# Kernel tuning notes

Measured on AMD Instinct MI355X. Metric: run time of the kernel, lower is better.

The kernel has to match this reference:

```python
import jax, jax.numpy as jnp
import numpy as np

D_MODEL = 1024
D_STATE = 64
HEADDIM = 64
EXPAND = 2
D_INNER = D_MODEL * EXPAND          # 2048
NHEADS = D_INNER // HEADDIM          # 32
D_IN_PROJ = 2 * D_INNER + 2 * D_STATE + NHEADS  # 4256
BATCH, SEQLEN = 4, 4096


def layernorm(x, w, b, eps=1e-5):
    mu = jnp.mean(x, axis=-1, keepdims=True)
    var = jnp.mean(jnp.square(x - mu), axis=-1, keepdims=True)
    return (x - mu) * jax.lax.rsqrt(var + eps) * w + b


def setup_inputs() -> dict:
    key = jax.random.key(0)
    ks = jax.random.split(key, 5)
    x = jax.random.normal(ks[0], (BATCH, SEQLEN, D_MODEL), dtype=jnp.float32)
    # xavier-ish small init (gain 0.5) as in _init_weights
    in_proj_w = jax.random.normal(ks[1], (D_IN_PROJ, D_MODEL), dtype=jnp.float32) * 0.5 * np.sqrt(2.0 / (D_IN_PROJ + D_MODEL))
    out_proj_w = jax.random.normal(ks[2], (D_MODEL, D_INNER), dtype=jnp.float32) * 0.5 * np.sqrt(2.0 / (D_MODEL + D_INNER))
    A_log = jnp.log(jnp.arange(1, NHEADS + 1, dtype=jnp.float32))
    dt_bias = jax.random.normal(ks[3], (NHEADS,), dtype=jnp.float32) * 0.01 + 0.1
    Dparam = jnp.ones((NHEADS,), dtype=jnp.float32)
    return {
        'x': x, 'in_proj_w': in_proj_w, 'out_proj_w': out_proj_w,
        'A_log': A_log, 'dt_bias': dt_bias, 'Dparam': Dparam,
        'ln_w': jnp.ones((D_INNER,), jnp.float32), 'ln_b': jnp.zeros((D_INNER,), jnp.float32),
        'ni_w': jnp.ones((D_MODEL,), jnp.float32), 'ni_b': jnp.zeros((D_MODEL,), jnp.float32),
        'no_w': jnp.ones((D_MODEL,), jnp.float32), 'no_b': jnp.zeros((D_MODEL,), jnp.float32),
    }


def _selective_scan(x_multi, A, Bm, Cm, dt):
    # x_multi: [B,L,H,P], A: [H], Bm/Cm: [B,L,N], dt: [B,L,H]
    Bb, L, H, P = x_multi.shape
    N = Bm.shape[-1]
    dA = jnp.minimum(jnp.exp(dt * A[None, None, :]), 0.99)  # [B,L,H]

    def step(h, inp):
        x_t, B_t, C_t, dA_t = inp  # [B,H,P], [B,N], [B,N], [B,H]
        dBx = jnp.einsum('bhp,bn->bhpn', x_t, B_t)
        h = jnp.clip(dA_t[:, :, None, None] * h + dBx, -10.0, 10.0)
        y_t = jnp.einsum('bn,bhpn->bhp', C_t, h)
        return h, y_t

    h0 = jnp.zeros((Bb, H, P, N), dtype=x_multi.dtype)
    xs = (jnp.moveaxis(x_multi, 1, 0), jnp.moveaxis(Bm, 1, 0),
          jnp.moveaxis(Cm, 1, 0), jnp.moveaxis(dA, 1, 0))
    _, y = jax.lax.scan(step, h0, xs)  # y: [L,B,H,P]
    return jnp.moveaxis(y, 0, 1)


def reference(x, in_proj_w, out_proj_w, A_log, dt_bias, Dparam,
              ln_w, ln_b, ni_w, ni_b, no_w, no_b):
    Bb, L, Dm = x.shape
    x_norm = layernorm(x, ni_w, ni_b)
    zxbcdt = jnp.einsum('bld,ed->ble', x_norm, in_proj_w)  # [B,L,D_IN_PROJ]
    z = zxbcdt[..., :D_INNER]
    x_ssm = zxbcdt[..., D_INNER:2 * D_INNER]
    Bm = zxbcdt[..., 2 * D_INNER:2 * D_INNER + D_STATE]
    Cm = zxbcdt[..., 2 * D_INNER + D_STATE:2 * D_INNER + 2 * D_STATE]
    dt = zxbcdt[..., 2 * D_INNER + 2 * D_STATE:]
    dt = jnp.clip(jax.nn.softplus(dt + dt_bias[None, None, :]), 0.001, 0.1)  # [B,L,H]
    A = -jnp.exp(A_log)  # [H]
    x_multi = x_ssm.reshape(Bb, L, NHEADS, HEADDIM)
    y = _selective_scan(x_multi, A, Bm, Cm, dt)  # [B,L,H,P]
    y = y + x_multi * Dparam[None, None, :, None]  # D skip
    y = y.reshape(Bb, L, D_INNER)
    y = y * jax.nn.silu(z)
    y = layernorm(y, ln_w, ln_b)
    y = jnp.einsum('ble,de->bld', y, out_proj_w)
    y = jnp.clip(y, -10.0, 10.0)
    y = layernorm(y, no_w, no_b)
    return y
```

## Files before the change

### kernel.cpp

```cpp
#include <hip/hip_runtime.h>
#include <hip/hip_bf16.h>
#include <stdint.h>

typedef _Float16 F16;
typedef F16 f16x8 __attribute__((ext_vector_type(8)));
typedef F16 f16x4 __attribute__((ext_vector_type(4)));
typedef float f32x4 __attribute__((ext_vector_type(4)));

#define NTOK   16384
#define DMODEL 1024
#define DINNER 2048
#define DSTATE 64
#define NHEADS 32
#define DINPRJ 4256
#define SEQLEN_ 4096
#define SEGLEN 128
#define NSEG   32

__device__ __forceinline__ void load_lds16(const void* g, void* l) {
  __builtin_amdgcn_global_load_lds((__attribute__((address_space(1))) void*)g,
                                   (__attribute__((address_space(3))) void*)l,
                                   16, 0, 0);
}

__device__ __forceinline__ void lds_st8(F16* base, int row, int col, int rowbytes, f16x8 v) {
  int by = (row * rowbytes + col * 2) ^ ((row & 7) << 4);
  *(f16x8*)((char*)base + by) = v;
}
__device__ __forceinline__ void lds_st1(F16* base, int row, int col, int rowbytes, F16 v) {
  int by = (row * rowbytes + col * 2) ^ ((row & 7) << 4);
  *(F16*)((char*)base + by) = v;
}
__device__ __forceinline__ f16x8 lds_ld8(const F16* base, int row, int col, int rowbytes) {
  int by = (row * rowbytes + col * 2) ^ ((row & 7) << 4);
  return *(const f16x8*)((const char*)base + by);
}

__global__ __launch_bounds__(256) void cvt_kernel(const float* __restrict__ src,
                                                  F16* __restrict__ dst, int n4) {
  int i = blockIdx.x * 256 + threadIdx.x;
  if (i >= n4) return;
  float4 v = *(const float4*)(src + (size_t)i * 4);
  f16x4 o = { (F16)v.x, (F16)v.y, (F16)v.z, (F16)v.w };
  *(f16x4*)(dst + (size_t)i * 4) = o;
}

__device__ __forceinline__ void blk_reduce2(float& s, float& ss) {
  __shared__ float red[8];
#pragma unroll
  for (int m = 32; m >= 1; m >>= 1) { s += __shfl_xor(s, m, 64); ss += __shfl_xor(ss, m, 64); }
  int tid = threadIdx.x, wv = tid >> 6;
  if ((tid & 63) == 0) { red[wv * 2] = s; red[wv * 2 + 1] = ss; }
  __syncthreads();
  s  = red[0] + red[2] + red[4] + red[6];
  ss = red[1] + red[3] + red[5] + red[7];
}

__global__ __launch_bounds__(256) void ln_in_kernel(const float* __restrict__ x,
                                                    const float* __restrict__ w,
                                                    const float* __restrict__ b,
                                                    F16* __restrict__ out) {
  int row = blockIdx.x, tid = threadIdx.x;
  const float* xr = x + (size_t)row * DMODEL + tid * 4;
  float4 v = *(const float4*)xr;
  float s = v.x + v.y + v.z + v.w;
  float ss = v.x * v.x + v.y * v.y + v.z * v.z + v.w * v.w;
  blk_reduce2(s, ss);
  float mu = s * (1.f / DMODEL);
  float var = ss * (1.f / DMODEL) - mu * mu;
  float rs = rsqrtf(var + 1e-5f);
  float4 wv = *(const float4*)(w + tid * 4);
  float4 bv = *(const float4*)(b + tid * 4);
  f16x4 o;
  o.x = (F16)((v.x - mu) * rs * wv.x + bv.x);
  o.y = (F16)((v.y - mu) * rs * wv.y + bv.y);
  o.z = (F16)((v.z - mu) * rs * wv.z + bv.z);
  o.w = (F16)((v.w - mu) * rs * wv.w + bv.w);
  *(f16x4*)(out + (size_t)row * DMODEL + tid * 4) = o;
}

template<int KD, int EPI>
__global__ __launch_bounds__(256)
void gemm_kernel(const F16* __restrict__ A, const F16* __restrict__ W, int Nw,
                 F16* __restrict__ Z, F16* __restrict__ XS,
                 float* __restrict__ BC, float* __restrict__ DT,
                 float* __restrict__ O1)
{
  __shared__ __align__(16) F16 Alds[128 * 32];
  __shared__ __align__(16) F16 Blds[128 * 32];
  const int tid = threadIdx.x;
  const int lane = tid & 63;
  const int wid = tid >> 6;
  const int wm = wid >> 1, wn = wid & 1;
  const int m0 = blockIdx.x * 128, n0 = blockIdx.y * 128;
  const int lr = lane & 15, lk = lane >> 4;

  f32x4 acc[4][4];
#pragma unroll
  for (int i = 0; i < 4; ++i)
#pragma unroll
    for (int j = 0; j < 4; ++j) acc[i][j] = f32x4{0.f, 0.f, 0.f, 0.f};

  const int srow = tid >> 2;
  const int scol = (tid & 3) * 8;
  const size_t arow0 = (size_t)(m0 + srow) * KD + scol;
  const size_t arow1 = (size_t)(m0 + srow + 64) * KD + scol;
  int wr0 = n0 + srow;      if (wr0 >= Nw) wr0 = Nw - 1;
  int wr1 = n0 + srow + 64; if (wr1 >= Nw) wr1 = Nw - 1;
  const size_t brow0 = (size_t)wr0 * KD + scol;
  const size_t brow1 = (size_t)wr1 * KD + scol;

  for (int k0 = 0; k0 < KD; k0 += 32) {
    load_lds16(A + arow0 + k0, &Alds[tid * 8]);
    load_lds16(A + arow1 + k0, &Alds[tid * 8 + 2048]);
    load_lds16(W + brow0 + k0, &Blds[tid * 8]);
    load_lds16(W + brow1 + k0, &Blds[tid * 8 + 2048]);
    __syncthreads();
    f16x8 af[4], bfr[4];
#pragma unroll
    for (int m = 0; m < 4; ++m)
      af[m] = *(const f16x8*)&Alds[(wm * 64 + m * 16 + lr) * 32 + lk * 8];
#pragma unroll
    for (int n = 0; n < 4; ++n)
      bfr[n] = *(const f16x8*)&Blds[(wn * 64 + n * 16 + lr) * 32 + lk * 8];
#pragma unroll
    for (int m = 0; m < 4; ++m)
#pragma unroll
      for (int n = 0; n < 4; ++n)
        acc[m][n] = __builtin_amdgcn_mfma_f32_16x16x32_f16(af[m], bfr[n], acc[m][n], 0, 0, 0);
    __syncthreads();
  }

#pragma unroll
  for (int m = 0; m < 4; ++m) {
#pragma unroll
    for (int n = 0; n < 4; ++n) {
      int r0 = m0 + wm * 64 + m * 16 + lk * 4;
      int c  = n0 + wn * 64 + n * 16 + lr;
#pragma unroll
      for (int j = 0; j < 4; ++j) {
        float v = acc[m][n][j];
        size_t r = (size_t)(r0 + j);
        if (EPI == 1) {
          O1[r * 1024 + c] = v;
        } else {
          if (c < 2048)        Z[r * 2048 + c] = (F16)v;
          else if (c < 4096)   XS[r * 2048 + (c - 2048)] = (F16)v;
          else if (c < 4160)   BC[r * 128 + (c - 4096)] = v;
          else if (c < 4224)   BC[r * 128 + 64 + (c - 4160)] = v;
          else if (c < 4256)   DT[r * 32 + (c - 4224)] = v;
        }
      }
    }
  }
}

__global__ __launch_bounds__(256) void da_kernel(float* __restrict__ dtraw,
                                                 const float* __restrict__ dt_bias,
                                                 const float* __restrict__ A_log) {
  int idx = blockIdx.x * 256 + threadIdx.x;
  int h = idx & 31;
  float v = dtraw[idx] + dt_bias[h];
  float sp = (v > 20.f) ? v : log1pf(expf(v));
  float dt = fminf(fmaxf(sp, 0.001f), 0.1f);
  float Ah = -expf(A_log[h]);
  dtraw[idx] = fminf(dt * Ah, -0.01005034f);
}

__global__ __launch_bounds__(128) void la_kernel(const float* __restrict__ LD,
                                                 float* __restrict__ LA) {
  const int bh = blockIdx.x, seg = blockIdx.y;
  const int b = bh >> 5, h = bh & 31;
  const int t = threadIdx.x, lane = t & 63;
  size_t tok = (size_t)b * SEQLEN_ + (size_t)seg * SEGLEN + t;
  float v = LD[tok * 32 + h];
#pragma unroll
  for (int m = 1; m <= 32; m <<= 1) {
    float o = __shfl_up(v, m, 64);
    if (lane >= m) v += o;
  }
  __shared__ float w0tot;
  if (t == 63) w0tot = v;
  __syncthreads();
  if (t >= 64) v += w0tot;
  LA[(size_t)bh * SEQLEN_ + (size_t)seg * SEGLEN + t] = v;
}

__global__ __launch_bounds__(256) void ssd_kernel(const float* __restrict__ BC,
                                                  const float* __restrict__ LA,
                                                  F16* __restrict__ XS,
                                                  const float* __restrict__ Dparam,
                                                  F16* __restrict__ HLOC) {
  __shared__ __align__(16) F16 Cb[128 * 64];
  __shared__ __align__(16) F16 Bb[128 * 64];
  __shared__ __align__(16) F16 Xb[64 * 128];
  __shared__ __align__(16) F16 Mm[128 * 128];
  const int h = blockIdx.x, seg = blockIdx.y, b = blockIdx.z;
  const int tid = threadIdx.x, lane = tid & 63, w = tid >> 6;
  const int lr = lane & 15, lk = lane >> 4;
  const int bh = b * 32 + h;
  const size_t tok0 = (size_t)b * SEQLEN_ + (size_t)seg * SEGLEN;
  const float* la = LA + (size_t)bh * SEQLEN_ + (size_t)seg * SEGLEN;

  {
    const int t = tid >> 1, half = tid & 1;
    const float* srcB = BC + (tok0 + t) * 128 + half * 32;
    const float* srcC = srcB + 64;
#pragma unroll
    for (int i = 0; i < 4; ++i) {
      float4 b0 = *(const float4*)(srcB + i * 8);
      float4 b1 = *(const float4*)(srcB + i * 8 + 4);
      float4 c0 = *(const float4*)(srcC + i * 8);
      float4 c1 = *(const float4*)(srcC + i * 8 + 4);
      f16x8 bo = { (F16)b0.x, (F16)b0.y, (F16)b0.z, (F16)b0.w,
                   (F16)b1.x, (F16)b1.y, (F16)b1.z, (F16)b1.w };
      f16x8 co = { (F16)c0.x, (F16)c0.y, (F16)c0.z, (F16)c0.w,
                   (F16)c1.x, (F16)c1.y, (F16)c1.z, (F16)c1.w };
      lds_st8(Bb, t, half * 32 + i * 8, 128, bo);
      lds_st8(Cb, t, half * 32 + i * 8, 128, co);
    }
  }
#pragma unroll
  for (int pass = 0; pass < 4; ++pass) {
    const int srel = tid & 31, oct = tid >> 5;
    const int s = pass * 32 + srel;
    f16x8 xv = *(const f16x8*)(XS + (tok0 + s) * 2048 + h * 64 + oct * 8);
#pragma unroll
    for (int i = 0; i < 8; ++i)
      lds_st1(Xb, oct * 8 + i, s, 256, xv[i]);
  }
  __syncthreads();

  f32x4 g[2][8];
#pragma unroll
  for (int m = 0; m < 2; ++m)
#pragma unroll
    for (int n = 0; n < 8; ++n) g[m][n] = f32x4{0.f, 0.f, 0.f, 0.f};
#pragma unroll
  for (int kk = 0; kk < 2; ++kk) {
    f16x8 a0 = lds_ld8(Cb, w * 32 + lr,      kk * 32 + lk * 8, 128);
    f16x8 a1 = lds_ld8(Cb, w * 32 + 16 + lr, kk * 32 + lk * 8, 128);
#pragma unroll
    for (int n = 0; n < 8; ++n) {
      f16x8 bq = lds_ld8(Bb, n * 16 + lr, kk * 32 + lk * 8, 128);
      g[0][n] = __builtin_amdgcn_mfma_f32_16x16x32_f16(a0, bq, g[0][n], 0, 0, 0);
      g[1][n] = __builtin_amdgcn_mfma_f32_16x16x32_f16(a1, bq, g[1][n], 0, 0, 0);
    }
  }
  const float Dh = Dparam[h];
  float lat[2][4];
#pragma unroll
  for (int m = 0; m < 2; ++m)
#pragma unroll
    for (int j = 0; j < 4; ++j)
      lat[m][j] = la[w * 32 + m * 16 + lk * 4 + j];
#pragma unroll
  for (int n = 0; n < 8; ++n) {
    const int s = n * 16 + lr;
    const float las = la[s];
#pragma unroll
    for (int m = 0; m < 2; ++m)
#pragma unroll
      for (int j = 0; j < 4; ++j) {
        const int t = w * 32 + m * 16 + lk * 4 + j;
        float v = (s <= t) ? g[m][n][j] * __expf(lat[m][j] - las) : 0.f;
        if (s == t) v += Dh;
        lds_st1(Mm, t, s, 256, (F16)v);
      }
  }
  __syncthreads();

  f32x4 y[2][4];
#pragma unroll
  for (int m = 0; m < 2; ++m)
#pragma unroll
    for (int n = 0; n < 4; ++n) y[m][n] = f32x4{0.f, 0.f, 0.f, 0.f};
#pragma unroll
  for (int kk = 0; kk < 4; ++kk) {
    f16x8 a0 = lds_ld8(Mm, w * 32 + lr,      kk * 32 + lk * 8, 256);
    f16x8 a1 = lds_ld8(Mm, w * 32 + 16 + lr, kk * 32 + lk * 8, 256);
#pragma unroll
    for (int n = 0; n < 4; ++n) {
      f16x8 bq = lds_ld8(Xb, n * 16 + lr, kk * 32 + lk * 8, 256);
      y[0][n] = __builtin_amdgcn_mfma_f32_16x16x32_f16(a0, bq, y[0][n], 0, 0, 0);
      y[1][n] = __builtin_amdgcn_mfma_f32_16x16x32_f16(a1, bq, y[1][n], 0, 0, 0);
    }
  }
#pragma unroll
  for (int m = 0; m < 2; ++m)
#pragma unroll
    for (int n = 0; n < 4; ++n)
#pragma unroll
      for (int j = 0; j < 4; ++j) {
        const int t = w * 32 + m * 16 + lk * 4 + j;
        const int p = n * 16 + lr;
        XS[(tok0 + t) * 2048 + h * 64 + p] = (F16)y[m][n][j];
      }
  __syncthreads();

  {
    const int s = tid >> 1, half = tid & 1;
    const float dec = __expf(la[127] - la[s]);
    const float* srcB = BC + (tok0 + s) * 128 + half * 32;
#pragma unroll
    for (int i = 0; i < 4; ++i) {
      float4 b0 = *(const float4*)(srcB + i * 8);
      float4 b1 = *(const float4*)(srcB + i * 8 + 4);
      float vv[8] = { b0.x, b0.y, b0.z, b0.w, b1.x, b1.y, b1.z, b1.w };
#pragma unroll
      for (int q = 0; q < 8; ++q)
        lds_st1(Mm, half * 32 + i * 8 + q, s, 256, (F16)(vv[q] * dec));
    }
  }
  __syncthreads();

  f32x4 hh[4];
#pragma unroll
  for (int n = 0; n < 4; ++n) hh[n] = f32x4{0.f, 0.f, 0.f, 0.f};
#pragma unroll
  for (int kk = 0; kk < 4; ++kk) {
    f16x8 a = lds_ld8(Xb, w * 16 + lr, kk * 32 + lk * 8, 256);
#pragma unroll
    for (int n = 0; n < 4; ++n) {
      f16x8 bq = lds_ld8(Mm, n * 16 + lr, kk * 32 + lk * 8, 256);
      hh[n] = __builtin_amdgcn_mfma_f32_16x16x32_f16(a, bq, hh[n], 0, 0, 0);
    }
  }
  F16* dst = HLOC + ((size_t)bh * NSEG + seg) * 4096;
#pragma unroll
  for (int n = 0; n < 4; ++n)
#pragma unroll
    for (int j = 0; j < 4; ++j) {
      const int p = w * 16 + lk * 4 + j;
      dst[p * 64 + n * 16 + lr] = (F16)hh[n][j];
    }
}

__global__ __launch_bounds__(256) void combine_kernel(F16* __restrict__ HLOC,
                                                      const float* __restrict__ LA) {
  const int bh = blockIdx.x, tid = threadIdx.x;
  const int p = tid >> 2, n0 = (tid & 3) * 16;
  F16* base = HLOC + (size_t)bh * NSEG * 4096 + p * 64 + n0;
  const float* la = LA + (size_t)bh * SEQLEN_;
  union U16 { uint4 v[2]; F16 h[16]; };
  float r[16];
#pragma unroll
  for (int i = 0; i < 16; ++i) r[i] = 0.f;
  for (int k = 0; k < NSEG; ++k) {
    F16* slot = base + (size_t)k * 4096;
    U16 hl; hl.v[0] = *(const uint4*)slot; hl.v[1] = *((const uint4*)slot + 1);
    float P = __expf(la[k * SEGLEN + SEGLEN - 1]);
    U16 ob;
#pragma unroll
    for (int i = 0; i < 16; ++i) ob.h[i] = (F16)r[i];
    *(uint4*)slot = ob.v[0]; *((uint4*)slot + 1) = ob.v[1];
#pragma unroll
    for (int i = 0; i < 16; ++i) r[i] = fmaf(P, r[i], (float)hl.h[i]);
  }
}

__global__ __launch_bounds__(256) void corr_kernel(const float* __restrict__ BC,
                                                   const float* __restrict__ LA,
                                                   const F16* __restrict__ HLOC,
                                                   F16* __restrict__ XS) {
  __shared__ __align__(16) F16 Cd[128 * 72];
  __shared__ __align__(16) F16 Hb[64 * 72];
  const int seg = blockIdx.x, h = blockIdx.y, b = blockIdx.z;
  const int tid = threadIdx.x;
  const size_t tok0 = (size_t)b * SEQLEN_ + (size_t)seg * SEGLEN;
  const int bh = b * 32 + h;
  {
    int t = tid >> 1, half = tid & 1;
    float Dv = __expf(LA[(size_t)bh * SEQLEN_ + seg * SEGLEN + t]);
    const float* src = BC + (tok0 + t) * 128 + 64 + half * 32;
    F16* dstp = &Cd[t * 72 + half * 32];
#pragma unroll
    for (int i = 0; i < 4; ++i) {
      float4 v0 = *(const float4*)(src + i * 8);
      float4 v1 = *(const float4*)(src + i * 8 + 4);
      f16x8 o = { (F16)(Dv * v0.x), (F16)(Dv * v0.y), (F16)(Dv * v0.z), (F16)(Dv * v0.w),
                  (F16)(Dv * v1.x), (F16)(Dv * v1.y), (F16)(Dv * v1.z), (F16)(Dv * v1.w) };
      *(f16x8*)(dstp + i * 8) = o;
    }
  }
  {
    int p = tid >> 2, nn = (tid & 3) * 16;
    const F16* src = HLOC + ((size_t)bh * NSEG + seg) * 4096 + p * 64 + nn;
    uint4 a0 = *(const uint4*)src, a1 = *((const uint4*)src + 1);
    *(uint4*)&Hb[p * 72 + nn] = a0;
    *(uint4*)&Hb[p * 72 + nn + 8] = a1;
  }
  __syncthreads();
  const int lane = tid & 63, w = tid >> 6;
  const int lr = lane & 15, lk = lane >> 4;
  f32x4 acc[2][4];
#pragma unroll
  for (int m = 0; m < 2; ++m)
#pragma unroll
    for (int n = 0; n < 4; ++n) acc[m][n] = f32x4{0.f, 0.f, 0.f, 0.f};
#pragma unroll
  for (int kk = 0; kk < 2; ++kk) {
    f16x8 a0 = *(const f16x8*)&Cd[(w * 32 + lr) * 72 + kk * 32 + lk * 8];
    f16x8 a1 = *(const f16x8*)&Cd[(w * 32 + 16 + lr) * 72 + kk * 32 + lk * 8];
#pragma unroll
    for (int n = 0; n < 4; ++n) {
      f16x8 bq = *(const f16x8*)&Hb[(n * 16 + lr) * 72 + kk * 32 + lk * 8];
      acc[0][n] = __builtin_amdgcn_mfma_f32_16x16x32_f16(a0, bq, acc[0][n], 0, 0, 0);
      acc[1][n] = __builtin_amdgcn_mfma_f32_16x16x32_f16(a1, bq, acc[1][n], 0, 0, 0);
    }
  }
#pragma unroll
  for (int m = 0; m < 2; ++m)
#pragma unroll
    for (int n = 0; n < 4; ++n)
#pragma unroll
      for (int j = 0; j < 4; ++j) {
        int t = w * 32 + m * 16 + lk * 4 + j;
        int p = n * 16 + lr;
        F16* yp = XS + (tok0 + t) * 2048 + h * 64 + p;
        *yp = (F16)((float)*yp + acc[m][n][j]);
      }
}

__global__ __launch_bounds__(256) void silu_ln_kernel(F16* __restrict__ Y,
                                                      const F16* __restrict__ Z,
                                                      const float* __restrict__ lnw,
                                                      const float* __restrict__ lnb) {
  int row = blockIdx.x, tid = threadIdx.x;
  size_t base = (size_t)row * DINNER + tid * 8;
  union { uint4 v; F16 h[8]; } yb, zb, ob;
  yb.v = *(const uint4*)(Y + base);
  zb.v = *(const uint4*)(Z + base);
  float vv[8];
  float s = 0.f, ss = 0.f;
#pragma unroll
  for (int i = 0; i < 8; ++i) {
    float y = (float)yb.h[i];
    float z = (float)zb.h[i];
    float sg = 1.f / (1.f + expf(-z));
    float v = y * z * sg;
    vv[i] = v; s += v; ss += v * v;
  }
  blk_reduce2(s, ss);
  float mu = s * (1.f / DINNER);
  float var = ss * (1.f / DINNER) - mu * mu;
  float rs = rsqrtf(var + 1e-5f);
#pragma unroll
  for (int i = 0; i < 8; ++i) {
    float w = lnw[tid * 8 + i], b = lnb[tid * 8 + i];
    ob.h[i] = (F16)((vv[i] - mu) * rs * w + b);
  }
  *(uint4*)(Y + base) = ob.v;
}

__global__ __launch_bounds__(256) void final_ln_kernel(float* __restrict__ O1,
                                                       const float* __restrict__ w,
                                                       const float* __restrict__ b) {
  int row = blockIdx.x, tid = threadIdx.x;
  size_t base = (size_t)row * DMODEL + tid * 4;
  float4 v = *(const float4*)(O1 + base);
  v.x = fminf(fmaxf(v.x, -10.f), 10.f);
  v.y = fminf(fmaxf(v.y, -10.f), 10.f);
  v.z = fminf(fmaxf(v.z, -10.f), 10.f);
  v.w = fminf(fmaxf(v.w, -10.f), 10.f);
  float s = v.x + v.y + v.z + v.w;
  float ss = v.x * v.x + v.y * v.y + v.z * v.z + v.w * v.w;
  blk_reduce2(s, ss);
  float mu = s * (1.f / DMODEL);
  float var = ss * (1.f / DMODEL) - mu * mu;
  float rs = rsqrtf(var + 1e-5f);
  float4 wv = *(const float4*)(w + tid * 4);
  float4 bv = *(const float4*)(b + tid * 4);
  float4 o;
  o.x = (v.x - mu) * rs * wv.x + bv.x;
  o.y = (v.y - mu) * rs * wv.y + bv.y;
  o.z = (v.z - mu) * rs * wv.z + bv.z;
  o.w = (v.w - mu) * rs * wv.w + bv.w;
  *(float4*)(O1 + base) = o;
}

extern "C" void kernel_launch(void* const* d_in, const int* in_sizes, int n_in,
                              void* d_out, int out_size, void* d_ws, size_t ws_size,
                              hipStream_t stream) {
  const float* x       = (const float*)d_in[0];
  const float* w1      = (const float*)d_in[1];
  const float* w2      = (const float*)d_in[2];
  const float* A_log   = (const float*)d_in[3];
  const float* dt_bias = (const float*)d_in[4];
  const float* Dparam  = (const float*)d_in[5];
  const float* ln_w    = (const float*)d_in[6];
  const float* ln_b    = (const float*)d_in[7];
  const float* ni_w    = (const float*)d_in[8];
  const float* ni_b    = (const float*)d_in[9];
  const float* no_w    = (const float*)d_in[10];
  const float* no_b    = (const float*)d_in[11];

  const size_t NEEDED = 119865344ull;
  if (ws_size < NEEDED) return;

  char* wsb = (char*)d_ws;
  F16*   XS   = (F16*)  (wsb + 0ull);
  float* BC   = (float*)(wsb + 67108864ull);
  float* DT   = (float*)(wsb + 75497472ull);
  F16*   XN   = (F16*)  (wsb + 77594624ull);
  F16*   W2F  = (F16*)  (wsb + 77594624ull);
  F16*   HLOC = (F16*)  (wsb + 81788928ull);
  float* LA   = (float*)(wsb + 115343360ull);
  F16*   W1F  = (F16*)  (wsb + 111149056ull);

  F16*   Z   = (F16*)d_out;
  float* O1  = (float*)d_out;

  cvt_kernel<<<4256, 256, 0, stream>>>(w1, W1F, (DINPRJ * DMODEL) / 4);
  ln_in_kernel<<<NTOK, 256, 0, stream>>>(x, ni_w, ni_b, XN);
  gemm_kernel<1024, 0><<<dim3(NTOK / 128, 34), 256, 0, stream>>>(
      XN, W1F, DINPRJ, Z, XS, BC, DT, nullptr);
  cvt_kernel<<<2048, 256, 0, stream>>>(w2, W2F, (DMODEL * DINNER) / 4);
  da_kernel<<<(NTOK * 32) / 256, 256, 0, stream>>>(DT, dt_bias, A_log);
  la_kernel<<<dim3(128, NSEG), 128, 0, stream>>>(DT, LA);
  ssd_kernel<<<dim3(32, NSEG, 4), 256, 0, stream>>>(BC, LA, XS, Dparam, HLOC);
  combine_kernel<<<128, 256, 0, stream>>>(HLOC, LA);
  corr_kernel<<<dim3(NSEG, 32, 4), 256, 0, stream>>>(BC, LA, HLOC, XS);
  silu_ln_kernel<<<NTOK, 256, 0, stream>>>(XS, Z, ln_w, ln_b);
  gemm_kernel<2048, 1><<<dim3(NTOK / 128, 8), 256, 0, stream>>>(
      XS, W2F, 1024, nullptr, nullptr, nullptr, nullptr, O1);
  final_ln_kernel<<<NTOK, 256, 0, stream>>>(O1, no_w, no_b);
}
```

Measured before the change: 587.6 us.

## Deepen GEMM K-tile to 64 with XOR-swizzled LDS and remapped block order

```diff
diff --git a/kernel.cpp b/kernel.cpp
--- a/kernel.cpp
+++ b/kernel.cpp
@@ -86,13 +86,16 @@
                  float* __restrict__ BC, float* __restrict__ DT,
                  float* __restrict__ O1)
 {
-  __shared__ __align__(16) F16 Alds[128 * 32];
-  __shared__ __align__(16) F16 Blds[128 * 32];
+  __shared__ __align__(16) F16 Alds[128 * 64];
+  __shared__ __align__(16) F16 Blds[128 * 64];
   const int tid = threadIdx.x;
   const int lane = tid & 63;
   const int wid = tid >> 6;
   const int wm = wid >> 1, wn = wid & 1;
-  const int m0 = blockIdx.x * 128, n0 = blockIdx.y * 128;
+  const int id = blockIdx.x;
+  const int bx = (id & 7) * 16 + ((id >> 3) & 15);
+  const int by = id >> 7;
+  const int m0 = bx * 128, n0 = by * 128;
   const int lr = lane & 15, lk = lane >> 4;
 
   f32x4 acc[4][4];
@@ -101,33 +104,33 @@
 #pragma unroll
     for (int j = 0; j < 4; ++j) acc[i][j] = f32x4{0.f, 0.f, 0.f, 0.f};
 
-  const int srow = tid >> 2;
-  const int scol = (tid & 3) * 8;
-  const size_t arow0 = (size_t)(m0 + srow) * KD + scol;
-  const size_t arow1 = (size_t)(m0 + srow + 64) * KD + scol;
-  int wr0 = n0 + srow;      if (wr0 >= Nw) wr0 = Nw - 1;
-  int wr1 = n0 + srow + 64; if (wr1 >= Nw) wr1 = Nw - 1;
-  const size_t brow0 = (size_t)wr0 * KD + scol;
-  const size_t brow1 = (size_t)wr1 * KD + scol;
-
-  for (int k0 = 0; k0 < KD; k0 += 32) {
-    load_lds16(A + arow0 + k0, &Alds[tid * 8]);
-    load_lds16(A + arow1 + k0, &Alds[tid * 8 + 2048]);
-    load_lds16(W + brow0 + k0, &Blds[tid * 8]);
-    load_lds16(W + brow1 + k0, &Blds[tid * 8 + 2048]);
+  for (int k0 = 0; k0 < KD; k0 += 64) {
+#pragma unroll
+    for (int it = 0; it < 4; ++it) {
+      const int q = it * 256 + tid;
+      const int row = q >> 3, c = q & 7;
+      const int cl = c ^ (row & 7);
+      load_lds16(A + (size_t)(m0 + row) * KD + k0 + cl * 8, &Alds[q * 8]);
+      int wr = n0 + row; if (wr >= Nw) wr = Nw - 1;
+      load_lds16(W + (size_t)wr * KD + k0 + cl * 8, &Blds[q * 8]);
+    }
     __syncthreads();
-    f16x8 af[4], bfr[4];
-#pragma unroll
-    for (int m = 0; m < 4; ++m)
-      af[m] = *(const f16x8*)&Alds[(wm * 64 + m * 16 + lr) * 32 + lk * 8];
-#pragma unroll
-    for (int n = 0; n < 4; ++n)
-      bfr[n] = *(const f16x8*)&Blds[(wn * 64 + n * 16 + lr) * 32 + lk * 8];
-#pragma unroll
-    for (int m = 0; m < 4; ++m)
+#pragma unroll
+    for (int kk = 0; kk < 2; ++kk) {
+      const int cs = ((kk * 4 + lk) ^ (lr & 7)) * 8;
+      f16x8 af[4], bfr[4];
+#pragma unroll
+      for (int m = 0; m < 4; ++m)
+        af[m] = *(const f16x8*)&Alds[(wm * 64 + m * 16 + lr) * 64 + cs];
 #pragma unroll
       for (int n = 0; n < 4; ++n)
-        acc[m][n] = __builtin_amdgcn_mfma_f32_16x16x32_f16(af[m], bfr[n], acc[m][n], 0, 0, 0);
+        bfr[n] = *(const f16x8*)&Blds[(wn * 64 + n * 16 + lr) * 64 + cs];
+#pragma unroll
+      for (int m = 0; m < 4; ++m)
+#pragma unroll
+        for (int n = 0; n < 4; ++n)
+          acc[m][n] = __builtin_amdgcn_mfma_f32_16x16x32_f16(af[m], bfr[n], acc[m][n], 0, 0, 0);
+    }
     __syncthreads();
   }
 
@@ -513,7 +516,7 @@
 
   cvt_kernel<<<4256, 256, 0, stream>>>(w1, W1F, (DINPRJ * DMODEL) / 4);
   ln_in_kernel<<<NTOK, 256, 0, stream>>>(x, ni_w, ni_b, XN);
-  gemm_kernel<1024, 0><<<dim3(NTOK / 128, 34), 256, 0, stream>>>(
+  gemm_kernel<1024, 0><<<128 * 34, 256, 0, stream>>>(
       XN, W1F, DINPRJ, Z, XS, BC, DT, nullptr);
   cvt_kernel<<<2048, 256, 0, stream>>>(w2, W2F, (DMODEL * DINNER) / 4);
   da_kernel<<<(NTOK * 32) / 256, 256, 0, stream>>>(DT, dt_bias, A_log);
@@ -522,7 +525,7 @@
   combine_kernel<<<128, 256, 0, stream>>>(HLOC, LA);
   corr_kernel<<<dim3(NSEG, 32, 4), 256, 0, stream>>>(BC, LA, HLOC, XS);
   silu_ln_kernel<<<NTOK, 256, 0, stream>>>(XS, Z, ln_w, ln_b);
-  gemm_kernel<2048, 1><<<dim3(NTOK / 128, 8), 256, 0, stream>>>(
+  gemm_kernel<2048, 1><<<128 * 8, 256, 0, stream>>>(
       XS, W2F, 1024, nullptr, nullptr, nullptr, nullptr, O1);
   final_ln_kernel<<<NTOK, 256, 0, stream>>>(O1, no_w, no_b);
 }
```

Measured after the change: 544.2 us. 1.08x faster.
